# Kernel tuning notes

Measured on AMD Instinct MI355X. Metric: run time of the kernel, lower is better.

The kernel has to match this reference:

```python
import jax, jax.numpy as jnp
import numpy as np

D_HEAD = 64  # per-head dim 'd' from init_kwargs


def layer_norm(x, g, b, eps=1e-5):
    m = x.mean(-1, keepdims=True)
    v = x.var(-1, keepdims=True)  # biased var, matches torch LayerNorm
    return (x - m) / jnp.sqrt(v + eps) * g + b


def setup_inputs() -> dict:
    key = jax.random.key(0)
    ks = jax.random.split(key, 16)
    F = 512
    B, T, N = 2, 8, 1024
    s = 1.0 / np.sqrt(F)
    u = lambda k, shape: jax.random.uniform(k, shape, jnp.float32, -s, s)
    return {
        "x": jax.random.normal(ks[0], (B, T, N, F), jnp.float32),
        "Wq": u(ks[1], (F, F)), "bq": u(ks[2], (F,)),
        "Wk": u(ks[3], (F, F)), "bk": u(ks[4], (F,)),
        "Wv": u(ks[5], (F, F)), "bv": u(ks[6], (F,)),
        "ln_g": jnp.ones((F,), jnp.float32), "ln_b": jnp.zeros((F,), jnp.float32),
        "W1": u(ks[7], (F, F)), "b1": u(ks[8], (F,)),
        "W2": u(ks[9], (F, F)), "b2": u(ks[10], (F,)),
        "lnff_g": jnp.ones((F,), jnp.float32), "lnff_b": jnp.zeros((F,), jnp.float32),
    }


def reference(x, Wq, bq, Wk, bk, Wv, bv, ln_g, ln_b, W1, b1, W2, b2, lnff_g, lnff_b):
    B, T, N, F = x.shape
    h = F // D_HEAD
    # q/k/v projections
    q = x @ Wq + bq
    k = x @ Wk + bk
    v = x @ Wv + bv
    # split last dim into heads (split+cat(dim=0) in torch == head axis here)
    qh = q.reshape(B, T, N, h, D_HEAD)
    kh = k.reshape(B, T, N, h, D_HEAD)
    vh = v.reshape(B, T, N, h, D_HEAD)
    # attention over node axis N per (batch, time, head)
    A = jnp.einsum('btqhd,btkhd->bthqk', qh, kh) / jnp.sqrt(jnp.asarray(D_HEAD, x.dtype))
    A = jax.nn.softmax(A, axis=-1)
    o = jnp.einsum('bthqk,btkhd->btqhd', A, vh).reshape(B, T, N, F)
    # residual + LN
    val = layer_norm(o + x, ln_g, ln_b)
    # FFN + final LN
    ff = jax.nn.relu(val @ W1 + b1) @ W2 + b2
    return layer_norm(ff, lnff_g, lnff_b)
```

## Files before the change

kernel.cpp:

```cpp
#include <hip/hip_runtime.h>
#include <hip/hip_bf16.h>

using bf16 = __hip_bfloat16;
typedef unsigned int u32x4 __attribute__((ext_vector_type(4)));
typedef float f32x4 __attribute__((ext_vector_type(4)));
typedef __bf16 bf16x8 __attribute__((ext_vector_type(8)));

#define DEVI __device__ __forceinline__

DEVI f32x4 mfma16(u32x4 a, u32x4 b, f32x4 c) {
    return __builtin_amdgcn_mfma_f32_16x16x32_bf16(
        __builtin_bit_cast(bf16x8, a), __builtin_bit_cast(bf16x8, b), c, 0, 0, 0);
}

DEVI void gload16(const bf16* g, bf16* l) {
    __builtin_amdgcn_global_load_lds(
        (const __attribute__((address_space(1))) unsigned int*)g,
        (__attribute__((address_space(3))) unsigned int*)l,
        16, 0, 0);
}

struct bf8 { bf16 h[8]; };

DEVI u32x4 pack8(f32x4 lo, f32x4 hi) {
    bf8 t;
#pragma unroll
    for (int i = 0; i < 4; i++) {
        t.h[i] = __float2bfloat16(lo[i]);
        t.h[4 + i] = __float2bfloat16(hi[i]);
    }
    return __builtin_bit_cast(u32x4, t);
}

DEVI unsigned long long pk4(float a, float b, float c, float d) {
    union { unsigned long long u; bf16 h[4]; } t;
    t.h[0] = __float2bfloat16(a); t.h[1] = __float2bfloat16(b);
    t.h[2] = __float2bfloat16(c); t.h[3] = __float2bfloat16(d);
    return t.u;
}

DEVI unsigned trunc2(float a, float b) {
    return __builtin_amdgcn_perm(__builtin_bit_cast(unsigned, b),
                                 __builtin_bit_cast(unsigned, a), 0x07060302);
}

__global__ __launch_bounds__(256) void prep(
    const float* __restrict__ Wq, const float* __restrict__ Wk,
    const float* __restrict__ Wv, const float* __restrict__ W1,
    const float* __restrict__ W2, const float* __restrict__ x,
    bf16* __restrict__ WT, bf16* __restrict__ xb)
{
    int b = blockIdx.x;
    if (b < 5120) {
        int w = b >> 10;
        const float* src = (w == 0) ? Wq : (w == 1) ? Wk : (w == 2) ? Wv : (w == 3) ? W1 : W2;
        int idx = (b & 1023) * 256 + threadIdx.x;
        int n = idx >> 9, kk = idx & 511;
        WT[(size_t)w * 262144 + idx] = __float2bfloat16(src[kk * 512 + n]);
    } else {
        size_t i = ((size_t)(b - 5120) * 256 + threadIdx.x) * 8;
        f32x4 lo = *(const f32x4*)&x[i];
        f32x4 hi = *(const f32x4*)&x[i + 4];
        *(u32x4*)&xb[i] = pack8(lo, hi);
    }
}

#define GEMM_BODY(EPILOGUE)                                                          \
    __shared__ __align__(16) bf16 As[128 * 64];                                      \
    __shared__ __align__(16) bf16 Bs[128 * 64];                                      \
    const int tid = threadIdx.x;                                                     \
    const int lane = tid & 63, wave = tid >> 6;                                      \
    const int wm = (wave >> 1) * 64, wn = (wave & 1) * 64;                           \
    const int lm = lane & 15, lq = lane >> 4;                                        \
    const int cxor = (lm & 7) * 8;                                                   \
    const int srow = wave * 32 + (lane >> 3);                                        \
    const int scol = ((lane & 7) ^ (lane >> 3)) * 8;                                 \
    const bf16* Ag = A + (size_t)(bm + srow) * 512 + scol;                           \
    const bf16* Bg = Bt + (size_t)(bn + srow) * 512 + scol;                          \
    bf16* Al = &As[wave * 32 * 64];                                                  \
    bf16* Bl = &Bs[wave * 32 * 64];                                                  \
    f32x4 acc[4][4];                                                                 \
    _Pragma("unroll") for (int i = 0; i < 4; i++)                                    \
        _Pragma("unroll") for (int j = 0; j < 4; j++)                                \
            acc[i][j] = (f32x4){0.f, 0.f, 0.f, 0.f};                                 \
    for (int k0 = 0; k0 < 512; k0 += 64) {                                           \
        __syncthreads();                                                             \
        _Pragma("unroll") for (int p = 0; p < 4; p++) {                              \
            gload16(Ag + (size_t)p * 8 * 512 + k0, Al + p * 512);                    \
            gload16(Bg + (size_t)p * 8 * 512 + k0, Bl + p * 512);                    \
        }                                                                            \
        __syncthreads();                                                             \
        _Pragma("unroll") for (int h = 0; h < 2; h++) {                              \
            u32x4 af[4], bfr[4];                                                     \
            _Pragma("unroll") for (int i = 0; i < 4; i++)                            \
                af[i] = *(const u32x4*)&As[(wm + i * 16 + lm) * 64 + ((h * 32 + lq * 8) ^ cxor)]; \
            _Pragma("unroll") for (int j = 0; j < 4; j++)                            \
                bfr[j] = *(const u32x4*)&Bs[(wn + j * 16 + lm) * 64 + ((h * 32 + lq * 8) ^ cxor)]; \
            EPILOGUE##_MMA                                                           \
        }                                                                            \
    }

#define SWAPPED_MMA                                                                  \
    _Pragma("unroll") for (int i = 0; i < 4; i++)                                    \
        _Pragma("unroll") for (int j = 0; j < 4; j++)                                \
            acc[i][j] = mfma16(bfr[j], af[i], acc[i][j]);

#define GEMM_BODY_N64(EPILOGUE)                                                      \
    __shared__ __align__(16) bf16 As[128 * 64];                                      \
    __shared__ __align__(16) bf16 Bs[64 * 64];                                       \
    const int tid = threadIdx.x;                                                     \
    const int lane = tid & 63, wave = tid >> 6;                                      \
    const int wm = wave * 32;                                                        \
    const int lm = lane & 15, lq = lane >> 4;                                        \
    const int cxor = (lm & 7) * 8;                                                   \
    const int sr8 = lane >> 3;                                                       \
    const int scol = ((lane & 7) ^ sr8) * 8;                                         \
    const bf16* Ag = A + (size_t)(bm + wave * 32 + sr8) * 512 + scol;                \
    const bf16* Bg = Bt + (size_t)(bn + wave * 16 + sr8) * 512 + scol;               \
    bf16* Al = &As[wave * 32 * 64];                                                  \
    bf16* Bl = &Bs[wave * 16 * 64];                                                  \
    f32x4 acc[2][4];                                                                 \
    _Pragma("unroll") for (int i = 0; i < 2; i++)                                    \
        _Pragma("unroll") for (int j = 0; j < 4; j++)                                \
            acc[i][j] = (f32x4){0.f, 0.f, 0.f, 0.f};                                 \
    for (int k0 = 0; k0 < 512; k0 += 64) {                                           \
        __syncthreads();                                                             \
        _Pragma("unroll") for (int p = 0; p < 4; p++)                                \
            gload16(Ag + (size_t)p * 8 * 512 + k0, Al + p * 512);                    \
        _Pragma("unroll") for (int p = 0; p < 2; p++)                                \
            gload16(Bg + (size_t)p * 8 * 512 + k0, Bl + p * 512);                    \
        __syncthreads();                                                             \
        _Pragma("unroll") for (int h = 0; h < 2; h++) {                              \
            u32x4 af[2], bfr[4];                                                     \
            _Pragma("unroll") for (int i = 0; i < 2; i++)                            \
                af[i] = *(const u32x4*)&As[(wm + i * 16 + lm) * 64 + ((h * 32 + lq * 8) ^ cxor)]; \
            _Pragma("unroll") for (int j = 0; j < 4; j++)                            \
                bfr[j] = *(const u32x4*)&Bs[(j * 16 + lm) * 64 + ((h * 32 + lq * 8) ^ cxor)]; \
            EPILOGUE##_MMA_N64                                                       \
        }                                                                            \
    }

#define SWAPPED_MMA_N64                                                              \
    _Pragma("unroll") for (int i = 0; i < 2; i++)                                    \
        _Pragma("unroll") for (int j = 0; j < 4; j++)                                \
            acc[i][j] = mfma16(bfr[j], af[i], acc[i][j]);
#define NORMAL_MMA_N64                                                               \
    _Pragma("unroll") for (int i = 0; i < 2; i++)                                    \
        _Pragma("unroll") for (int j = 0; j < 4; j++)                                \
            acc[i][j] = mfma16(af[i], bfr[j], acc[i][j]);

__global__ __launch_bounds__(256) void gemm_qk(
    const bf16* __restrict__ A, const bf16* __restrict__ WT,
    const float* __restrict__ bqp, const float* __restrict__ bkp,
    bf16* __restrict__ qb, bf16* __restrict__ kb)
{
    const int wsel = blockIdx.y >> 2;
    const int bm = blockIdx.x * 128, bn = (blockIdx.y & 3) * 128;
    const bf16* Bt = WT + (size_t)wsel * 262144;
    const float* bias = (wsel == 0) ? bqp : bkp;
    const float scale = (wsel == 0) ? 0.18033688f : 1.0f;
    bf16* dst = (wsel == 0) ? qb : kb;

    GEMM_BODY(SWAPPED)
#pragma unroll
    for (int i = 0; i < 4; i++) {
#pragma unroll
        for (int j = 0; j < 4; j++) {
            int row = bm + wm + i * 16 + lm;
            int colb = bn + wn + j * 16 + lq * 4;
            f32x4 b4 = *(const f32x4*)&bias[colb];
            *(unsigned long long*)&dst[(size_t)row * 512 + colb] =
                pk4((acc[i][j][0] + b4[0]) * scale, (acc[i][j][1] + b4[1]) * scale,
                    (acc[i][j][2] + b4[2]) * scale, (acc[i][j][3] + b4[3]) * scale);
        }
    }
}

__global__ __launch_bounds__(256) void gemm_v(
    const bf16* __restrict__ A, const bf16* __restrict__ WT,
    const float* __restrict__ bvp, bf16* __restrict__ vT)
{
    const int bm = blockIdx.x * 128, bn = blockIdx.y * 64;
    const bf16* Bt = WT + (size_t)2 * 262144;
    const float* bias = bvp;

    GEMM_BODY_N64(NORMAL)
#pragma unroll
    for (int i = 0; i < 2; i++) {
#pragma unroll
        for (int j = 0; j < 4; j++) {
            int col = bn + j * 16 + lm;
            float bv = bias[col];
            int rowb = bm + wm + i * 16 + lq * 4;
            int btq = rowb >> 10, node = rowb & 1023;
            int u = node & 31;
            int nodeP = (node & ~31) | (((u >> 2) & 3) << 3) | (((u >> 4) & 1) << 2);
            *(unsigned long long*)&vT[((size_t)((btq * 8 + (col >> 6)) * 64 + (col & 63))) * 1024 + nodeP] =
                pk4(acc[i][j][0] + bv, acc[i][j][1] + bv,
                    acc[i][j][2] + bv, acc[i][j][3] + bv);
        }
    }
}

template <bool RELU>
__global__ __launch_bounds__(256) void gemm_bt(
    const bf16* __restrict__ A, const bf16* __restrict__ Bt,
    const float* __restrict__ bias, bf16* __restrict__ C)
{
    const int bm = blockIdx.x * 128, bn = blockIdx.y * 64;
    GEMM_BODY_N64(SWAPPED)
#pragma unroll
    for (int i = 0; i < 2; i++) {
#pragma unroll
        for (int j = 0; j < 4; j++) {
            int row = bm + wm + i * 16 + lm;
            int colb = bn + j * 16 + lq * 4;
            f32x4 b4 = *(const f32x4*)&bias[colb];
            float c0 = acc[i][j][0] + b4[0], c1 = acc[i][j][1] + b4[1];
            float c2 = acc[i][j][2] + b4[2], c3 = acc[i][j][3] + b4[3];
            if (RELU) {
                c0 = fmaxf(c0, 0.f); c1 = fmaxf(c1, 0.f);
                c2 = fmaxf(c2, 0.f); c3 = fmaxf(c3, 0.f);
            }
            *(unsigned long long*)&C[(size_t)row * 512 + colb] = pk4(c0, c1, c2, c3);
        }
    }
}

__global__ __launch_bounds__(256, 4) void attn_kernel(
    const bf16* __restrict__ q, const bf16* __restrict__ k,
    const bf16* __restrict__ vT, bf16* __restrict__ o)
{
    constexpr int KP = 72;
    constexpr int VP = 72;
    __shared__ __align__(16) bf16 Ks[2][64 * KP];
    __shared__ __align__(16) bf16 Vs[2][64 * VP];

    const int tid = threadIdx.x, lane = tid & 63, wave = tid >> 6;
    const int group = blockIdx.x;
    const int bt = group >> 3, hh = group & 7;
    const int lm = lane & 15, lq = lane >> 4;
    const int qrow0 = bt * 1024 + blockIdx.y * 128 + wave * 32;

    u32x4 qf[2][2];
#pragma unroll
    for (int tm = 0; tm < 2; tm++)
#pragma unroll
        for (int kk2 = 0; kk2 < 2; kk2++)
            qf[tm][kk2] = *(const u32x4*)&q[(size_t)(qrow0 + tm * 16 + lm) * 512 + hh * 64 + kk2 * 32 + lq * 8];

    const bf16* kbase = k + (size_t)(bt * 1024) * 512 + hh * 64;
    const bf16* vbase = vT + (size_t)group * 64 * 1024;

    const int r0 = tid >> 3, e0 = (tid & 7) * 8;
    const int r1 = (256 + tid) >> 3;

    const unsigned ow = (lm == 0) ? 0x3F803F80u : 0u;
    const u32x4 onesA = (u32x4){ow, ow, ow, ow};

    f32x4 accO[4][2];
#pragma unroll
    for (int md = 0; md < 4; md++)
#pragma unroll
        for (int tm = 0; tm < 2; tm++) accO[md][tm] = (f32x4){0.f, 0.f, 0.f, 0.f};
    f32x4 accL[2] = {(f32x4){0.f, 0.f, 0.f, 0.f}, (f32x4){0.f, 0.f, 0.f, 0.f}};

    u32x4 kreg0 = *(const u32x4*)&kbase[(size_t)r0 * 512 + e0];
    u32x4 kreg1 = *(const u32x4*)&kbase[(size_t)r1 * 512 + e0];
    u32x4 vreg0 = *(const u32x4*)&vbase[(size_t)r0 * 1024 + e0];
    u32x4 vreg1 = *(const u32x4*)&vbase[(size_t)r1 * 1024 + e0];

    for (int kt = 0; kt < 16; kt++) {
        bf16* Kb = Ks[kt & 1];
        bf16* Vb = Vs[kt & 1];
        *(u32x4*)&Kb[r0 * KP + e0] = kreg0;
        *(u32x4*)&Kb[r1 * KP + e0] = kreg1;
        *(u32x4*)&Vb[r0 * VP + e0] = vreg0;
        *(u32x4*)&Vb[r1 * VP + e0] = vreg1;
        __syncthreads();
        if (kt < 15) {
            const bf16* kn = kbase + (size_t)((kt + 1) * 64) * 512;
            const bf16* vn = vbase + (kt + 1) * 64;
            kreg0 = *(const u32x4*)&kn[(size_t)r0 * 512 + e0];
            kreg1 = *(const u32x4*)&kn[(size_t)r1 * 512 + e0];
            vreg0 = *(const u32x4*)&vn[(size_t)r0 * 1024 + e0];
            vreg1 = *(const u32x4*)&vn[(size_t)r1 * 1024 + e0];
        }

#pragma unroll
        for (int kc = 0; kc < 2; kc++) {
            const int t0 = kc * 2;
            u32x4 kf00 = *(const u32x4*)&Kb[(t0 * 16 + lm) * KP + lq * 8];
            u32x4 kf01 = *(const u32x4*)&Kb[(t0 * 16 + lm) * KP + 32 + lq * 8];
            u32x4 kf10 = *(const u32x4*)&Kb[((t0 + 1) * 16 + lm) * KP + lq * 8];
            u32x4 kf11 = *(const u32x4*)&Kb[((t0 + 1) * 16 + lm) * KP + 32 + lq * 8];
            u32x4 pw[2];
#pragma unroll
            for (int tm = 0; tm < 2; tm++) {
                f32x4 s0 = (f32x4){0.f, 0.f, 0.f, 0.f};
                s0 = mfma16(kf00, qf[tm][0], s0);
                s0 = mfma16(kf01, qf[tm][1], s0);
                f32x4 s1 = (f32x4){0.f, 0.f, 0.f, 0.f};
                s1 = mfma16(kf10, qf[tm][0], s1);
                s1 = mfma16(kf11, qf[tm][1], s1);
                float p0 = __builtin_amdgcn_exp2f(s0[0]);
                float p1 = __builtin_amdgcn_exp2f(s0[1]);
                float p2 = __builtin_amdgcn_exp2f(s0[2]);
                float p3 = __builtin_amdgcn_exp2f(s0[3]);
                float p4 = __builtin_amdgcn_exp2f(s1[0]);
                float p5 = __builtin_amdgcn_exp2f(s1[1]);
                float p6 = __builtin_amdgcn_exp2f(s1[2]);
                float p7 = __builtin_amdgcn_exp2f(s1[3]);
                pw[tm] = (u32x4){trunc2(p0, p1), trunc2(p2, p3),
                                 trunc2(p4, p5), trunc2(p6, p7)};
            }
            accL[0] = mfma16(onesA, pw[0], accL[0]);
            accL[1] = mfma16(onesA, pw[1], accL[1]);
            __builtin_amdgcn_s_setprio(1);
#pragma unroll
            for (int md = 0; md < 4; md++) {
                u32x4 vf = *(const u32x4*)&Vb[(md * 16 + lm) * VP + kc * 32 + lq * 8];
                accO[md][0] = mfma16(vf, pw[0], accO[md][0]);
                accO[md][1] = mfma16(vf, pw[1], accO[md][1]);
            }
            __builtin_amdgcn_s_setprio(0);
        }
    }

#pragma unroll
    for (int tm = 0; tm < 2; tm++) {
        float l = accL[tm][0];
        l += __shfl_xor(l, 16);
        l += __shfl_xor(l, 32);
        float linv = 1.0f / l;
#pragma unroll
        for (int md = 0; md < 4; md++) {
            *(unsigned long long*)&o[(size_t)(qrow0 + tm * 16 + lm) * 512 + hh * 64 + md * 16 + lq * 4] =
                pk4(accO[md][tm][0] * linv, accO[md][tm][1] * linv,
                    accO[md][tm][2] * linv, accO[md][tm][3] * linv);
        }
    }
}

template <bool AF32, bool RES, bool OF32>
__global__ __launch_bounds__(256) void ln_kernel(
    const void* __restrict__ a, const float* __restrict__ res,
    const float* __restrict__ g, const float* __restrict__ bb, void* __restrict__ out)
{
    int row = blockIdx.x * 4 + (threadIdx.x >> 6);
    int lane = threadIdx.x & 63;
    size_t base = (size_t)row * 512 + lane * 8;
    int cbase = lane * 8;

    float x8[8];
    if (AF32) {
        const float* af = (const float*)a;
        f32x4 lo = *(const f32x4*)&af[base];
        f32x4 hi = *(const f32x4*)&af[base + 4];
#pragma unroll
        for (int i = 0; i < 4; i++) { x8[i] = lo[i]; x8[4 + i] = hi[i]; }
    } else {
        bf8 av = __builtin_bit_cast(bf8, *(const u32x4*)&((const bf16*)a)[base]);
#pragma unroll
        for (int i = 0; i < 8; i++) x8[i] = __bfloat162float(av.h[i]);
    }
    if (RES) {
        f32x4 lo = *(const f32x4*)&res[base];
        f32x4 hi = *(const f32x4*)&res[base + 4];
#pragma unroll
        for (int i = 0; i < 4; i++) { x8[i] += lo[i]; x8[4 + i] += hi[i]; }
    }

    float s = 0.f, s2 = 0.f;
#pragma unroll
    for (int i = 0; i < 8; i++) { s += x8[i]; s2 += x8[i] * x8[i]; }
#pragma unroll
    for (int off = 1; off < 64; off <<= 1) {
        s += __shfl_xor(s, off);
        s2 += __shfl_xor(s2, off);
    }
    float mean = s * (1.f / 512.f);
    float var = s2 * (1.f / 512.f) - mean * mean;
    float rstd = rsqrtf(var + 1e-5f);

    f32x4 g0 = *(const f32x4*)&g[cbase], g1 = *(const f32x4*)&g[cbase + 4];
    f32x4 b0 = *(const f32x4*)&bb[cbase], b1v = *(const f32x4*)&bb[cbase + 4];
    float y[8];
#pragma unroll
    for (int i = 0; i < 4; i++) {
        y[i] = (x8[i] - mean) * rstd * g0[i] + b0[i];
        y[4 + i] = (x8[4 + i] - mean) * rstd * g1[i] + b1v[i];
    }
    if (OF32) {
        float* op = (float*)out;
        *(f32x4*)&op[base] = (f32x4){y[0], y[1], y[2], y[3]};
        *(f32x4*)&op[base + 4] = (f32x4){y[4], y[5], y[6], y[7]};
    } else {
        bf8 ov;
#pragma unroll
        for (int i = 0; i < 8; i++) ov.h[i] = __float2bfloat16(y[i]);
        *(u32x4*)&((bf16*)out)[base] = __builtin_bit_cast(u32x4, ov);
    }
}

extern "C" void kernel_launch(void* const* d_in, const int* in_sizes, int n_in,
                              void* d_out, int out_size, void* d_ws, size_t ws_size,
                              hipStream_t stream)
{
    const float* x    = (const float*)d_in[0];
    const float* Wq   = (const float*)d_in[1];
    const float* bq   = (const float*)d_in[2];
    const float* Wk   = (const float*)d_in[3];
    const float* bk   = (const float*)d_in[4];
    const float* Wv   = (const float*)d_in[5];
    const float* bv   = (const float*)d_in[6];
    const float* ln_g = (const float*)d_in[7];
    const float* ln_b = (const float*)d_in[8];
    const float* W1   = (const float*)d_in[9];
    const float* b1   = (const float*)d_in[10];
    const float* W2   = (const float*)d_in[11];
    const float* b2   = (const float*)d_in[12];
    const float* lnffg = (const float*)d_in[13];
    const float* lnffb = (const float*)d_in[14];
    float* out = (float*)d_out;

    bf16* ws = (bf16*)d_ws;
    bf16* WT = ws;
    bf16* qb = ws + 5 * 262144;
    bf16* kb = qb + 8388608;
    bf16* vT = kb + 8388608;
    bf16* vl = qb;
    bf16* f1 = kb;
    bf16* f2 = vT;
    bf16* xb = (bf16*)d_out;
    bf16* ob = xb + 8388608;

    prep<<<9216, 256, 0, stream>>>(Wq, Wk, Wv, W1, W2, x, WT, xb);

    gemm_qk<<<dim3(128, 8), 256, 0, stream>>>(xb, WT, bq, bk, qb, kb);
    gemm_v <<<dim3(128, 8), 256, 0, stream>>>(xb, WT, bv, vT);

    attn_kernel<<<dim3(128, 8), 256, 0, stream>>>(qb, kb, vT, ob);

    ln_kernel<false, true, false><<<4096, 256, 0, stream>>>(ob, x, ln_g, ln_b, vl);

    dim3 gg(128, 8);
    gemm_bt<true> <<<gg, 256, 0, stream>>>(vl, WT + 3 * 262144, b1, f1);
    gemm_bt<false><<<gg, 256, 0, stream>>>(f1, WT + 4 * 262144, b2, f2);

    ln_kernel<false, false, true><<<4096, 256, 0, stream>>>(f2, nullptr, lnffg, lnffb, out);
}
```

Measured before the change: 244.3 us.

## Tile weight transpose through LDS and read bf16 residual in first LayerNorm

The weight prep kernel now transposes in 64x64 tiles staged through a padded shared-memory array, so both the global reads and the writes are coalesced. Before, each thread read a strided column element. A new LayerNorm kernel reads the residual from the bf16 copy of x instead of the fp32 input, which halves that read's traffic. The cost is residual precision: bf16-rounded x now feeds the residual add.

Result: no change. 239.7 us (-1.9%).

```diff
diff --git a/kernel.cpp b/kernel.cpp
--- a/kernel.cpp
+++ b/kernel.cpp
@@ -50,15 +50,29 @@
     const float* __restrict__ W2, const float* __restrict__ x,
     bf16* __restrict__ WT, bf16* __restrict__ xb)
 {
+    __shared__ float T[64][65];
     int b = blockIdx.x;
-    if (b < 5120) {
-        int w = b >> 10;
+    if (b < 320) {
+        int w = b >> 6;
+        int t = b & 63;
+        int kk0 = (t >> 3) * 64, n0 = (t & 7) * 64;
         const float* src = (w == 0) ? Wq : (w == 1) ? Wk : (w == 2) ? Wv : (w == 3) ? W1 : W2;
-        int idx = (b & 1023) * 256 + threadIdx.x;
-        int n = idx >> 9, kk = idx & 511;
-        WT[(size_t)w * 262144 + idx] = __float2bfloat16(src[kk * 512 + n]);
+        const int r4 = threadIdx.x >> 6;
+        const int c = threadIdx.x & 63;
+#pragma unroll
+        for (int p = 0; p < 16; p++) {
+            int row = p * 4 + r4;
+            T[row][c] = src[(size_t)(kk0 + row) * 512 + n0 + c];
+        }
+        __syncthreads();
+#pragma unroll
+        for (int p = 0; p < 16; p++) {
+            int nrow = p * 4 + r4;
+            WT[(size_t)w * 262144 + (size_t)(n0 + nrow) * 512 + kk0 + c] =
+                __float2bfloat16(T[c][nrow]);
+        }
     } else {
-        size_t i = ((size_t)(b - 5120) * 256 + threadIdx.x) * 8;
+        size_t i = ((size_t)(b - 320) * 256 + threadIdx.x) * 8;
         f32x4 lo = *(const f32x4*)&x[i];
         f32x4 hi = *(const f32x4*)&x[i + 4];
         *(u32x4*)&xb[i] = pack8(lo, hi);
@@ -342,6 +356,46 @@
     }
 }
 
+__global__ __launch_bounds__(256) void ln_bb(
+    const bf16* __restrict__ a, const bf16* __restrict__ res,
+    const float* __restrict__ g, const float* __restrict__ bb,
+    bf16* __restrict__ out)
+{
+    int row = blockIdx.x * 4 + (threadIdx.x >> 6);
+    int lane = threadIdx.x & 63;
+    size_t base = (size_t)row * 512 + lane * 8;
+    int cbase = lane * 8;
+
+    bf8 av = __builtin_bit_cast(bf8, *(const u32x4*)&a[base]);
+    bf8 rv = __builtin_bit_cast(bf8, *(const u32x4*)&res[base]);
+    float x8[8];
+#pragma unroll
+    for (int i = 0; i < 8; i++)
+        x8[i] = __bfloat162float(av.h[i]) + __bfloat162float(rv.h[i]);
+
+    float s = 0.f, s2 = 0.f;
+#pragma unroll
+    for (int i = 0; i < 8; i++) { s += x8[i]; s2 += x8[i] * x8[i]; }
+#pragma unroll
+    for (int off = 1; off < 64; off <<= 1) {
+        s += __shfl_xor(s, off);
+        s2 += __shfl_xor(s2, off);
+    }
+    float mean = s * (1.f / 512.f);
+    float var = s2 * (1.f / 512.f) - mean * mean;
+    float rstd = rsqrtf(var + 1e-5f);
+
+    f32x4 g0 = *(const f32x4*)&g[cbase], g1 = *(const f32x4*)&g[cbase + 4];
+    f32x4 b0 = *(const f32x4*)&bb[cbase], b1v = *(const f32x4*)&bb[cbase + 4];
+    bf8 ov;
+#pragma unroll
+    for (int i = 0; i < 4; i++) {
+        ov.h[i] = __float2bfloat16((x8[i] - mean) * rstd * g0[i] + b0[i]);
+        ov.h[4 + i] = __float2bfloat16((x8[4 + i] - mean) * rstd * g1[i] + b1v[i]);
+    }
+    *(u32x4*)&out[base] = __builtin_bit_cast(u32x4, ov);
+}
+
 template <bool AF32, bool RES, bool OF32>
 __global__ __launch_bounds__(256) void ln_kernel(
     const void* __restrict__ a, const float* __restrict__ res,
@@ -435,14 +489,14 @@
     bf16* xb = (bf16*)d_out;
     bf16* ob = xb + 8388608;
 
-    prep<<<9216, 256, 0, stream>>>(Wq, Wk, Wv, W1, W2, x, WT, xb);
+    prep<<<4416, 256, 0, stream>>>(Wq, Wk, Wv, W1, W2, x, WT, xb);
 
     gemm_qk<<<dim3(128, 8), 256, 0, stream>>>(xb, WT, bq, bk, qb, kb);
     gemm_v <<<dim3(128, 8), 256, 0, stream>>>(xb, WT, bv, vT);
 
     attn_kernel<<<dim3(128, 8), 256, 0, stream>>>(qb, kb, vT, ob);
 
-    ln_kernel<false, true, false><<<4096, 256, 0, stream>>>(ob, x, ln_g, ln_b, vl);
+    ln_bb<<<4096, 256, 0, stream>>>(ob, xb, ln_g, ln_b, vl);
 
     dim3 gg(128, 8);
     gemm_bt<true> <<<gg, 256, 0, stream>>>(vl, WT + 3 * 262144, b1, f1);
```
